# Kernel optimization log

Measured on AMD Instinct MI355X. Metric: run time of the kernel, lower is better.

Reference implementation:

```python
import jax, jax.numpy as jnp
import numpy as np

B, T, D_IN = 16, 4096, 512
D_EMB, N_CODES = 256, 1024


def setup_inputs() -> dict:
    key = jax.random.key(0)
    k1, k2, k3, k4 = jax.random.split(key, 4)
    z = jax.random.normal(k1, (B, T, D_IN), dtype=jnp.float32)
    embedding = jax.random.normal(k2, (N_CODES, D_EMB), dtype=jnp.float32)
    # torch Linear weight layout [out_features, in_features], bias=False
    proj_down_w = jax.random.normal(k3, (D_EMB, D_IN), dtype=jnp.float32) * (1.0 / np.sqrt(D_IN))
    proj_up_w = jax.random.normal(k4, (D_IN, D_EMB), dtype=jnp.float32) * (1.0 / np.sqrt(D_EMB))
    return {"z": z, "embedding": embedding, "proj_down_w": proj_down_w, "proj_up_w": proj_up_w}


def _quantize_to_code(z_e, codebook):
    # z_e: [b, t, d]; codebook: [n, d] -> indices [b, t]
    b, t, d = z_e.shape
    z_flat = z_e.reshape(b * t, d)
    dist = (jnp.sum(z_flat * z_flat, axis=1, keepdims=True)
            - 2.0 * (z_flat @ codebook.T)
            + jnp.sum(codebook * codebook, axis=1)[None, :])  # [(b t), n]
    return jnp.argmin(dist, axis=1).reshape(b, t)


def reference(z, embedding, proj_down_w, proj_up_w):
    # proj_down: z @ W_down^T
    z_e = jnp.einsum('btd,ed->bte', z, proj_down_w)  # [b, t, D_EMB]
    code = _quantize_to_code(z_e, embedding)
    z_q = embedding[code]  # gather: [b, t, D_EMB]
    diff2 = (z_q - z_e) ** 2
    commitment_loss = diff2.mean(axis=(1, 2))  # [b]
    codebook_loss = diff2.mean(axis=(1, 2))    # [b] (same values fwd; differ in grad)
    # straight-through estimator (training mode)
    z_q_st = z_e + jax.lax.stop_gradient(z_q - z_e)
    z_q_out = jnp.einsum('bte,de->btd', z_q_st, proj_up_w)  # [b, t, D_IN]
    return (z_q_out, commitment_loss, codebook_loss, code, z_e)
```

## Files before the change

### kernel.cpp

```cpp
#include <hip/hip_runtime.h>
#include <stdint.h>

#define DIN  512
#define DE   256
#define NC   1024
#define M_   65536
#define FLAGCAP 16384

typedef unsigned short u16;
typedef __attribute__((ext_vector_type(8))) short short8_t;
typedef __attribute__((ext_vector_type(4))) float f32x4_t;
typedef __attribute__((ext_vector_type(16))) float f32x16_t;

__device__ __forceinline__ float bf2f(u16 u) {
    unsigned x = ((unsigned)u) << 16; return __builtin_bit_cast(float, x);
}
__device__ __forceinline__ u16 f2bf(float f) {
    unsigned x = __builtin_bit_cast(unsigned, f);
    x += 0x7fffu + ((x >> 16) & 1u);
    return (u16)(x >> 16);
}
__device__ __forceinline__ void cvt8_hl(float4 a, float4 b, short8_t& h, short8_t& l) {
    float v[8] = {a.x,a.y,a.z,a.w, b.x,b.y,b.z,b.w};
#pragma unroll
    for (int j = 0; j < 8; ++j) {
        u16 hh = f2bf(v[j]);
        h[j] = (short)hh; l[j] = (short)f2bf(v[j] - bf2f(hh));
    }
}
__device__ __forceinline__ short8_t cvt8(float4 a, float4 b) {
    float v[8] = {a.x,a.y,a.z,a.w, b.x,b.y,b.z,b.w};
    short8_t h;
#pragma unroll
    for (int j = 0; j < 8; ++j) h[j] = (short)f2bf(v[j]);
    return h;
}

__global__ void k_init(const float* __restrict__ emb, const float* __restrict__ Wd,
                       u16* __restrict__ embH, u16* __restrict__ embL,
                       u16* __restrict__ WdH,  u16* __restrict__ WdL,
                       float* __restrict__ cnorm,
                       float* __restrict__ lossacc, int* __restrict__ flagcnt) {
    int tid = blockIdx.x * 256 + threadIdx.x;
    for (int i = tid; i < DE * DIN; i += 65536) {
        float v = Wd[i]; u16 h = f2bf(v);
        WdH[i] = h; WdL[i] = f2bf(v - bf2f(h));
    }
    for (int i = tid; i < NC * DE; i += 65536) {
        float v = emb[i]; u16 h = f2bf(v);
        embH[i] = h; embL[i] = f2bf(v - bf2f(h));
    }
    if (tid < NC) {
        const float* c = emb + (size_t)tid * DE;
        double s = 0.0;
        for (int j = 0; j < DE; ++j) { double v = c[j]; s += v * v; }
        cnorm[tid] = (float)s;
    }
    if (tid < 16) lossacc[tid] = 0.f;
    if (tid == 16) *flagcnt = 0;
}

__global__ __launch_bounds__(256, 2) void k_ze(
        const float* __restrict__ Z,
        const u16* __restrict__ WdH, const u16* __restrict__ WdL,
        float* __restrict__ zeF) {
    __shared__ __align__(16) u16 aH[2][128 * 40];
    __shared__ __align__(16) u16 aL[2][128 * 40];
    const int bz = blockIdx.x >> 1, mh = blockIdx.x & 1;
    const int m0 = bz * 128;
    const int nb = mh * 128;
    const int t = threadIdx.x, lane = t & 63, wv = t >> 6;
    const int lc = lane & 31, hi = lane >> 5;
    const int zsr = t >> 1, zss = (t & 1) * 16;
    const int wdrow = nb + wv * 32 + lc;
    const u16* WdHr = WdH + (size_t)wdrow * DIN;
    const u16* WdLr = WdL + (size_t)wdrow * DIN;

    float4 zf[4];
#define Z_LD(kt_) { \
        const float4* p = (const float4*)(Z + (size_t)(m0 + zsr) * DIN + (kt_) * 32 + zss); \
        zf[0] = p[0]; zf[1] = p[1]; zf[2] = p[2]; zf[3] = p[3]; }
#define Z_WR(b_) { \
        short8_t h0, l0, h1, l1; \
        cvt8_hl(zf[0], zf[1], h0, l0); cvt8_hl(zf[2], zf[3], h1, l1); \
        *(short8_t*)&aH[b_][zsr * 40 + zss]     = h0; \
        *(short8_t*)&aH[b_][zsr * 40 + zss + 8] = h1; \
        *(short8_t*)&aL[b_][zsr * 40 + zss]     = l0; \
        *(short8_t*)&aL[b_][zsr * 40 + zss + 8] = l1; }
#define WD_LD(kt_, H_, L_) { \
        H_[0] = *(const short8_t*)(WdHr + (kt_) * 32 + hi * 8); \
        H_[1] = *(const short8_t*)(WdHr + (kt_) * 32 + 16 + hi * 8); \
        L_[0] = *(const short8_t*)(WdLr + (kt_) * 32 + hi * 8); \
        L_[1] = *(const short8_t*)(WdLr + (kt_) * 32 + 16 + hi * 8); }

    short8_t wh[2], wl[2], nwh[2], nwl[2];
    Z_LD(0);
    WD_LD(0, wh, wl);
    Z_WR(0);
    __syncthreads();

    f32x16_t acc[4];
#pragma unroll
    for (int s = 0; s < 4; ++s)
#pragma unroll
        for (int r = 0; r < 16; ++r) acc[s][r] = 0.f;

    for (int kt = 0; kt < 16; ++kt) {
        if (kt < 15) { Z_LD(kt + 1); WD_LD(kt + 1, nwh, nwl); }
        const int buf = kt & 1;
#pragma unroll
        for (int ks = 0; ks < 2; ++ks) {
#pragma unroll
            for (int s = 0; s < 4; ++s) {
                const int lo = (s * 32 + lc) * 40 + ks * 16 + hi * 8;
                short8_t zh = *(const short8_t*)&aH[buf][lo];
                short8_t zl = *(const short8_t*)&aL[buf][lo];
                acc[s] = __builtin_amdgcn_mfma_f32_32x32x16_bf16(zh, wh[ks], acc[s], 0, 0, 0);
                acc[s] = __builtin_amdgcn_mfma_f32_32x32x16_bf16(zh, wl[ks], acc[s], 0, 0, 0);
                acc[s] = __builtin_amdgcn_mfma_f32_32x32x16_bf16(zl, wh[ks], acc[s], 0, 0, 0);
            }
        }
        if (kt < 15) {
            __syncthreads();
            Z_WR((kt + 1) & 1);
            wh[0] = nwh[0]; wh[1] = nwh[1];
            wl[0] = nwl[0]; wl[1] = nwl[1];
            __syncthreads();
        }
    }
#undef Z_LD
#undef Z_WR
#undef WD_LD

#pragma unroll
    for (int s = 0; s < 4; ++s)
#pragma unroll
        for (int r = 0; r < 16; ++r) {
            const int zr = m0 + s * 32 + (r & 3) + 8 * (r >> 2) + 4 * hi;
            zeF[(size_t)zr * DE + nb + wv * 32 + lc] = acc[s][r];
        }
}

__global__ __launch_bounds__(256, 2) void k_argmin(
        const float* __restrict__ zeF,
        const u16* __restrict__ embH, const u16* __restrict__ embL,
        const float* __restrict__ cnorm,
        u16* __restrict__ codew, int* __restrict__ flaglist,
        int* __restrict__ flagcnt, float* __restrict__ lossacc) {
    __shared__ __align__(16) u16 aH[2][128 * 40];
    __shared__ __align__(16) u16 aL[2][128 * 40];
    __shared__ float lCn[NC];
    __shared__ float lLoss[128];
    const int m0 = blockIdx.x * 128;
    const int t = threadIdx.x, lane = t & 63, wv = t >> 6;
    const int lc = lane & 31, hi = lane >> 5;
    const int zrow = m0 + wv * 32 + lc;

    for (int i = t; i < NC; i += 256) lCn[i] = cnorm[i];

    short8_t bh[16], bl[16];
    float rn = 0.f;
#pragma unroll
    for (int c = 0; c < 16; ++c) {
        const float4* zp = (const float4*)(zeF + (size_t)zrow * DE + c * 16 + hi * 8);
        float4 a = zp[0], b = zp[1];
        rn += a.x*a.x + a.y*a.y + a.z*a.z + a.w*a.w
            + b.x*b.x + b.y*b.y + b.z*b.z + b.w*b.w;
        cvt8_hl(a, b, bh[c], bl[c]);
    }
    rn += __shfl_xor(rn, 32, 64);

#define STAGE_E(ct_, kt_, b_) { \
        _Pragma("unroll") \
        for (int j = 0; j < 2; ++j) { \
            int idx = t + j * 256; \
            int row = idx >> 2, seg = (idx & 3) * 8; \
            size_t off = (size_t)((ct_) * 128 + row) * DE + (kt_) * 32 + seg; \
            uint4 vh = *(const uint4*)(embH + off); \
            uint4 vl = *(const uint4*)(embL + off); \
            *(uint4*)&aH[b_][row * 40 + seg] = vh; \
            *(uint4*)&aL[b_][row * 40 + seg] = vl; \
        } }

    float best = 3.4e38f, sec = 3.4e38f; int bidx = 0;
    STAGE_E(0, 0, 0);
    for (int ct = 0; ct < 8; ++ct) {
        f32x16_t acc[4];
#pragma unroll
        for (int s = 0; s < 4; ++s)
#pragma unroll
            for (int r = 0; r < 16; ++r) acc[s][r] = 0.f;
#pragma unroll
        for (int kt = 0; kt < 8; ++kt) {
            __syncthreads();
            if (kt < 7)      STAGE_E(ct, kt + 1, (kt + 1) & 1)
            else if (ct < 7) STAGE_E(ct + 1, 0, 0)
            const int buf = kt & 1;
#pragma unroll
            for (int ks = 0; ks < 2; ++ks) {
                const int c = kt * 2 + ks;
#pragma unroll
                for (int s = 0; s < 4; ++s) {
                    short8_t ah = *(const short8_t*)&aH[buf][(s * 32 + lc) * 40 + ks * 16 + hi * 8];
                    short8_t al = *(const short8_t*)&aL[buf][(s * 32 + lc) * 40 + ks * 16 + hi * 8];
                    acc[s] = __builtin_amdgcn_mfma_f32_32x32x16_bf16(ah, bh[c], acc[s], 0, 0, 0);
                    acc[s] = __builtin_amdgcn_mfma_f32_32x32x16_bf16(ah, bl[c], acc[s], 0, 0, 0);
                    acc[s] = __builtin_amdgcn_mfma_f32_32x32x16_bf16(al, bh[c], acc[s], 0, 0, 0);
                }
            }
        }
#pragma unroll
        for (int s = 0; s < 4; ++s)
#pragma unroll
            for (int r = 0; r < 16; ++r) {
                const int cidx = ct * 128 + s * 32 + (r & 3) + 8 * (r >> 2) + 4 * hi;
                float d = fmaf(-2.f, acc[s][r], lCn[cidx]);
                bool lt = d < best;
                sec  = lt ? best : fminf(sec, d);
                best = lt ? d : best;
                bidx = lt ? cidx : bidx;
            }
    }
#undef STAGE_E
    {
        float ob = __shfl_xor(best, 32, 64);
        float os = __shfl_xor(sec,  32, 64);
        int   oi = __shfl_xor(bidx, 32, 64);
        float ns = fminf(fminf(sec, os), fmaxf(best, ob));
        if (ob < best) { best = ob; bidx = oi; }
        sec = ns;
    }
    if (lane < 32) {
        codew[zrow] = (u16)bidx;
        if (sec - best < 0.02f) {
            int pos = atomicAdd(flagcnt, 1);
            if (pos < FLAGCAP) flaglist[pos] = zrow;
        }
        lLoss[wv * 32 + lc] = rn + best;
    }
    __syncthreads();
    for (int str = 64; str > 0; str >>= 1) {
        if (t < str) lLoss[t] += lLoss[t + str];
        __syncthreads();
    }
    if (t == 0) atomicAdd(&lossacc[m0 >> 12], lLoss[0]);
}

__global__ __launch_bounds__(256) void k_refine(
        const float* __restrict__ Z, const float* __restrict__ Wd,
        const float* __restrict__ emb,
        const int* __restrict__ flaglist, const int* __restrict__ flagcnt,
        u16* __restrict__ codew) {
    __shared__ float  lz[DIN];
    __shared__ double lze[DE];
    __shared__ double ld[256];
    __shared__ int    li[256];
    int n = *flagcnt; if (n < 0) n = 0; if (n > FLAGCAP) n = FLAGCAP;
    int t = threadIdx.x;
    for (int f = blockIdx.x; f < n; f += gridDim.x) {
        int row = flaglist[f] & (M_ - 1);
        __syncthreads();
        for (int i = t; i < DIN; i += 256) lz[i] = Z[(size_t)row * DIN + i];
        __syncthreads();
        double a = 0.0;
        const float* wr = Wd + (size_t)t * DIN;
        for (int k = 0; k < DIN; ++k) a += (double)lz[k] * (double)wr[k];
        lze[t] = a;
        __syncthreads();
        double bd = 1e300; int bi = 0;
        for (int cc = 0; cc < 4; ++cc) {
            int c = cc * 256 + t;
            const float* cr = emb + (size_t)c * DE;
            double s = 0.0;
            for (int e = 0; e < DE; ++e) {
                double diff = lze[e] - (double)cr[e];
                s += diff * diff;
            }
            if (s < bd) { bd = s; bi = c; }
        }
        ld[t] = bd; li[t] = bi;
        __syncthreads();
        for (int str = 128; str > 0; str >>= 1) {
            if (t < str) {
                double od = ld[t + str]; int oi = li[t + str];
                if (od < ld[t] || (od == ld[t] && oi < li[t])) { ld[t] = od; li[t] = oi; }
            }
            __syncthreads();
        }
        if (t == 0) codew[row] = (u16)li[0];
        __syncthreads();
    }
}

__global__ void k_loss(const float* __restrict__ lossacc,
                       float* __restrict__ out_commit, float* __restrict__ out_codebook) {
    int tid = threadIdx.x;
    if (tid < 16) {
        float v = lossacc[tid] * (1.f / 1048576.f);
        out_commit[tid] = v; out_codebook[tid] = v;
    }
}
__global__ void k_codef(const u16* __restrict__ codew, float* __restrict__ out_code) {
    int tid = blockIdx.x * 256 + threadIdx.x;
    if (tid < M_) out_code[tid] = (float)(codew[tid] & (NC - 1));
}

__global__ __launch_bounds__(512) void k_gemm3(
        const float* __restrict__ emb, const float* __restrict__ Wu,
        const float* __restrict__ out_code, float* __restrict__ out) {
    __shared__ __align__(16) u16 gA[128 * 264];
    const int bz = blockIdx.x >> 1, nh = blockIdx.x & 1;
    const int m0 = bz * 128;
    const int t = threadIdx.x, lane = t & 63, wv = t >> 6;
    const int lr = lane & 15, lg = lane >> 4;
    {
        const int row = t >> 2, seg = (t & 3) * 64;
        const int code = (int)out_code[m0 + row] & (NC - 1);
        const float* src = emb + (size_t)code * DE + seg;
#pragma unroll
        for (int j = 0; j < 8; ++j) {
            const float4* p = (const float4*)(src + j * 8);
            *(short8_t*)&gA[row * 264 + seg + j * 8] = cvt8(p[0], p[1]);
        }
    }
    __syncthreads();

    const int nbase = nh * 256 + wv * 32;
    f32x4_t acc[8][2];
#pragma unroll
    for (int i = 0; i < 8; ++i)
#pragma unroll
        for (int j = 0; j < 2; ++j) acc[i][j] = (f32x4_t){0.f, 0.f, 0.f, 0.f};

#pragma unroll
    for (int kt = 0; kt < 8; ++kt) {
        const int k0 = kt * 32 + lg * 8;
        short8_t b0, b1;
        {
            const float4* p = (const float4*)(Wu + (size_t)(nbase + lr) * DE + k0);
            b0 = cvt8(p[0], p[1]);
            const float4* q = (const float4*)(Wu + (size_t)(nbase + 16 + lr) * DE + k0);
            b1 = cvt8(q[0], q[1]);
        }
#pragma unroll
        for (int mi = 0; mi < 8; ++mi) {
            short8_t a = *(const short8_t*)&gA[(mi * 16 + lr) * 264 + k0];
            acc[mi][0] = __builtin_amdgcn_mfma_f32_16x16x32_bf16(a, b0, acc[mi][0], 0, 0, 0);
            acc[mi][1] = __builtin_amdgcn_mfma_f32_16x16x32_bf16(a, b1, acc[mi][1], 0, 0, 0);
        }
    }
#pragma unroll
    for (int mi = 0; mi < 8; ++mi)
#pragma unroll
        for (int reg = 0; reg < 4; ++reg) {
            const int zr = m0 + mi * 16 + lg * 4 + reg;
            out[(size_t)zr * DIN + nbase + lr]      = acc[mi][0][reg];
            out[(size_t)zr * DIN + nbase + 16 + lr] = acc[mi][1][reg];
        }
}

extern "C" void kernel_launch(void* const* d_in, const int* in_sizes, int n_in,
                              void* d_out, int out_size, void* d_ws, size_t ws_size,
                              hipStream_t stream) {
    const float* Z   = (const float*)d_in[0];
    const float* E   = (const float*)d_in[1];
    const float* Wd  = (const float*)d_in[2];
    const float* Wu  = (const float*)d_in[3];

    float* out       = (float*)d_out;
    float* out_zq    = out;
    float* out_com   = out + 33554432;
    float* out_cb    = out + 33554448;
    float* out_code  = out + 33554464;
    float* out_ze    = out + 33620000;

    char* scr = (char*)d_out;
    u16*   embH     = (u16*)  (scr + 0);
    u16*   embL     = (u16*)  (scr + 524288);
    u16*   WdH      = (u16*)  (scr + 1048576);
    u16*   WdL      = (u16*)  (scr + 1310720);
    float* cnorm    = (float*)(scr + 1572864);
    u16*   codew    = (u16*)  (scr + 1839104);
    int*   flaglist = (int*)  (scr + 1970176);
    int*   flagcnt  = (int*)  (scr + 2035712);
    float* lossacc  = (float*)(scr + 2035776);
    (void)d_ws; (void)ws_size; (void)in_sizes; (void)n_in; (void)out_size;

    k_init  <<<256,  256, 0, stream>>>(E, Wd, embH, embL, WdH, WdL, cnorm,
                                       lossacc, flagcnt);
    k_ze    <<<1024, 256, 0, stream>>>(Z, WdH, WdL, out_ze);
    k_argmin<<<512,  256, 0, stream>>>(out_ze, embH, embL, cnorm,
                                       codew, flaglist, flagcnt, lossacc);
    k_refine<<<128,  256, 0, stream>>>(Z, Wd, E, flaglist, flagcnt, codew);
    k_loss  <<<1,    64,  0, stream>>>(lossacc, out_com, out_cb);
    k_codef <<<256,  256, 0, stream>>>(codew, out_code);
    k_gemm3 <<<1024, 512, 0, stream>>>(E, Wu, out_code, out_zq);
}
```

Measured before the change: 362.5 us.

## Precompute codebook up-projection table and gather rows instead of final GEMM

```diff
diff --git a/kernel.cpp b/kernel.cpp
--- a/kernel.cpp
+++ b/kernel.cpp
@@ -58,6 +58,50 @@
     }
     if (tid < 16) lossacc[tid] = 0.f;
     if (tid == 16) *flagcnt = 0;
+}
+
+__global__ __launch_bounds__(256, 1) void k_pup(
+        const float* __restrict__ emb, const float* __restrict__ Wu,
+        float* __restrict__ P) {
+    __shared__ __align__(16) float le[64][260];
+    __shared__ __align__(16) float lw[64][260];
+    const int bi = blockIdx.x >> 3, bj = blockIdx.x & 7;
+    const int t = threadIdx.x;
+    {
+        const int r = t >> 2, q = (t & 3) * 64;
+        const float* se = emb + (size_t)(bi * 64 + r) * DE + q;
+        const float* sw = Wu  + (size_t)(bj * 64 + r) * DE + q;
+#pragma unroll
+        for (int i = 0; i < 16; ++i) {
+            *(float4*)&le[r][q + i * 4] = *(const float4*)(se + i * 4);
+            *(float4*)&lw[r][q + i * 4] = *(const float4*)(sw + i * 4);
+        }
+    }
+    __syncthreads();
+    const int ci = (t >> 4) * 4, oi = (t & 15) * 4;
+    float acc[4][4];
+#pragma unroll
+    for (int a = 0; a < 4; ++a)
+#pragma unroll
+        for (int b = 0; b < 4; ++b) acc[a][b] = 0.f;
+    for (int k = 0; k < DE; k += 4) {
+        float4 av[4], bv[4];
+#pragma unroll
+        for (int a = 0; a < 4; ++a) av[a] = *(const float4*)&le[ci + a][k];
+#pragma unroll
+        for (int b = 0; b < 4; ++b) bv[b] = *(const float4*)&lw[oi + b][k];
+#pragma unroll
+        for (int a = 0; a < 4; ++a)
+#pragma unroll
+            for (int b = 0; b < 4; ++b)
+                acc[a][b] += av[a].x * bv[b].x + av[a].y * bv[b].y
+                           + av[a].z * bv[b].z + av[a].w * bv[b].w;
+    }
+#pragma unroll
+    for (int a = 0; a < 4; ++a)
+#pragma unroll
+        for (int b = 0; b < 4; ++b)
+            P[(size_t)(bi * 64 + ci + a) * DIN + bj * 64 + oi + b] = acc[a][b];
 }
 
 __global__ __launch_bounds__(256, 2) void k_ze(
@@ -305,6 +349,19 @@
     if (tid < M_) out_code[tid] = (float)(codew[tid] & (NC - 1));
 }
 
+__global__ __launch_bounds__(256) void k_gather(
+        const float* __restrict__ P, const u16* __restrict__ codew,
+        float* __restrict__ out) {
+    const int g = blockIdx.x * 256 + threadIdx.x;
+    const float4* P4 = (const float4*)P;
+    float4* O4 = (float4*)out;
+    for (int u = g; u < M_ * 128; u += 524288) {
+        const int row = u >> 7, seg = u & 127;
+        const int c = codew[row] & (NC - 1);
+        O4[(size_t)row * 128 + seg] = P4[(size_t)c * 128 + seg];
+    }
+}
+
 __global__ __launch_bounds__(512) void k_gemm3(
         const float* __restrict__ emb, const float* __restrict__ Wu,
         const float* __restrict__ out_code, float* __restrict__ out) {
@@ -384,15 +441,23 @@
     int*   flaglist = (int*)  (scr + 1970176);
     int*   flagcnt  = (int*)  (scr + 2035712);
     float* lossacc  = (float*)(scr + 2035776);
-    (void)d_ws; (void)ws_size; (void)in_sizes; (void)n_in; (void)out_size;
+    (void)in_sizes; (void)n_in; (void)out_size;
+
+    const bool useP = (ws_size >= (size_t)NC * DIN * sizeof(float));
+    float* P = (float*)d_ws;
 
     k_init  <<<256,  256, 0, stream>>>(E, Wd, embH, embL, WdH, WdL, cnorm,
                                        lossacc, flagcnt);
+    if (useP)
+        k_pup <<<128, 256, 0, stream>>>(E, Wu, P);
     k_ze    <<<1024, 256, 0, stream>>>(Z, WdH, WdL, out_ze);
     k_argmin<<<512,  256, 0, stream>>>(out_ze, embH, embL, cnorm,
                                        codew, flaglist, flagcnt, lossacc);
     k_refine<<<128,  256, 0, stream>>>(Z, Wd, E, flaglist, flagcnt, codew);
     k_loss  <<<1,    64,  0, stream>>>(lossacc, out_com, out_cb);
     k_codef <<<256,  256, 0, stream>>>(codew, out_code);
-    k_gemm3 <<<1024, 512, 0, stream>>>(E, Wu, out_code, out_zq);
-}
+    if (useP)
+        k_gather<<<2048, 256, 0, stream>>>(P, codew, out_zq);
+    else
+        k_gemm3 <<<1024, 512, 0, stream>>>(E, Wu, out_code, out_zq);
+}
```

Result: faster. 353.2 us (-2.5%).
